# Optimization experiments

Hardware: AMD Instinct MI355X
Metric: run time of the kernel (lower is better)

## Reference

```python
import jax, jax.numpy as jnp
import numpy as np

WINDOW = 9       # attn_params.attention_window
DILATION = 1     # attn_params.attention_stride


def setup_inputs() -> dict:
    key = jax.random.key(0)
    kq, kk, kv = jax.random.split(key, 3)
    shape = (1, 8, 64, 64, 32)  # [B, heads, H, W, head_dim]
    return {
        "q": jax.random.normal(kq, shape, dtype=jnp.float32),
        "k": jax.random.normal(kk, shape, dtype=jnp.float32),
        "v": jax.random.normal(kv, shape, dtype=jnp.float32),
    }


def _neighborhood_attention_2d(q, k, v, K):
    """NATTEN-style 2D neighborhood attention, dilation=1, non-causal.

    Each query (i,j) attends to a KxK window of keys; at the borders the
    window is shifted (clamped) to stay fully inside the feature map,
    matching NATTEN semantics (no zero padding / masking).
    """
    B, h, H, W, D = q.shape
    half = K // 2
    # window start per row/col, clamped so the full window fits
    si = jnp.clip(jnp.arange(H) - half, 0, H - K)            # [H]
    sj = jnp.clip(jnp.arange(W) - half, 0, W - K)            # [W]
    ii = si[:, None] + jnp.arange(K)[None, :]                # [H, K]
    jj = sj[:, None] + jnp.arange(K)[None, :]                # [W, K]
    # gather neighborhoods: -> [B,h,H,K,W,K,D] -> [B,h,H,W,K,K,D]
    kn = jnp.transpose(k[:, :, ii][:, :, :, :, jj], (0, 1, 2, 4, 3, 5, 6))
    vn = jnp.transpose(v[:, :, ii][:, :, :, :, jj], (0, 1, 2, 4, 3, 5, 6))
    scale = 1.0 / jnp.sqrt(jnp.asarray(D, q.dtype))
    # logits over the KxK neighborhood
    logits = jnp.einsum('bhijd,bhijxyd->bhijxy', q * scale, kn)
    attn = jax.nn.softmax(logits.reshape(B, h, H, W, K * K), axis=-1)
    attn = attn.reshape(B, h, H, W, K, K)
    return jnp.einsum('bhijxy,bhijxyd->bhijd', attn, vn)


def reference(q, k, v):
    # mirror NA.forward: kernel_size = min(window, H, W), forced odd
    K = min(WINDOW, q.shape[2], q.shape[3])
    K -= 1 if K % 2 == 0 else 0
    return _neighborhood_attention_2d(q, k, v, K)
```

## Files before the change

kernel.cpp:

```cpp
#include <hip/hip_runtime.h>

#define HH 64
#define WW 64
#define DD 32
#define KW 9

typedef _Float16 f16;
typedef __attribute__((ext_vector_type(8))) _Float16 f16x8;
typedef __attribute__((ext_vector_type(4))) float f32x4;

__device__ __forceinline__ unsigned pk2(float lo, float hi) {
    unsigned short a = __builtin_bit_cast(unsigned short, (_Float16)lo);
    unsigned short b = __builtin_bit_cast(unsigned short, (_Float16)hi);
    return (unsigned)a | ((unsigned)b << 16);
}

__global__ __launch_bounds__(256) void na_attn_fused(
    const float* __restrict__ q, const float* __restrict__ k,
    const float* __restrict__ v, float* __restrict__ out)
{
    const int lane = threadIdx.x & 63;
    const int wv   = (blockIdx.x << 2) + (threadIdx.x >> 6);
    const int g    = lane >> 4;
    const int c16  = lane & 15;
    const int h  = wv >> 8;
    const int t  = wv & 255;
    const int i0 = (t >> 3) * 2;
    const int j0 = (t & 7) * 8;
    const int ry = min(max(i0 - 4, 0), HH - 10);
    const int rx = min(max(j0 - 4, 0), WW - 16);
    const int qi = i0 + (c16 >> 3);
    const int qj = j0 + (c16 & 7);
    const int si = min(max(qi - 4, 0), HH - KW);
    const int sj = min(max(qj - 4, 0), WW - KW);

    const int xb = rx + 4 * g;
    const bool cv0 = (unsigned)(xb + 0 - sj) < 9u;
    const bool cv1 = (unsigned)(xb + 1 - sj) < 9u;
    const bool cv2 = (unsigned)(xb + 2 - sj) < 9u;
    const bool cv3 = (unsigned)(xb + 3 - sj) < 9u;

    const float S = 0.17677669529663687f;
    const float* qp = q + (((size_t)h * HH + qi) * WW + qj) * DD + g * 8;
    f32x4 q0 = *(const f32x4*)qp;
    f32x4 q1 = *(const f32x4*)(qp + 4);
    union { unsigned u[4]; f16x8 h8; } Bq;
    Bq.u[0] = pk2(q0[0] * S, q0[1] * S);
    Bq.u[1] = pk2(q0[2] * S, q0[3] * S);
    Bq.u[2] = pk2(q1[0] * S, q1[1] * S);
    Bq.u[3] = pk2(q1[2] * S, q1[3] * S);

    const float* kbase = k + (((size_t)h * HH + ry) * WW + rx + c16) * DD + g * 8;
    const float* vbase = v + (((size_t)h * HH + (ry + (g >> 1))) * WW + rx + 8 * (g & 1)) * DD + c16;

    const int  sA  = c16 + ((g & 1) << 5);
    const int  sB  = sA + 16;
    const bool ghi = (g >= 2);

    f32x4 o0 = {0.f, 0.f, 0.f, 0.f};
    f32x4 o1 = {0.f, 0.f, 0.f, 0.f};
    const f32x4 zero = {0.f, 0.f, 0.f, 0.f};
    float lsum = 0.f;

#pragma unroll
    for (int cc = 0; cc < 5; ++cc) {
        const float* kp0 = kbase + (2 * cc) * (WW * DD);
        const float* kp1 = kp0 + (WW * DD);
        f32x4 ka = *(const f32x4*)kp0;
        f32x4 kb = *(const f32x4*)(kp0 + 4);
        f32x4 kc = *(const f32x4*)kp1;
        f32x4 kd = *(const f32x4*)(kp1 + 4);
        union { unsigned u[4]; f16x8 h8; } A0, A1;
        A0.u[0] = pk2(ka[0], ka[1]); A0.u[1] = pk2(ka[2], ka[3]);
        A0.u[2] = pk2(kb[0], kb[1]); A0.u[3] = pk2(kb[2], kb[3]);
        A1.u[0] = pk2(kc[0], kc[1]); A1.u[1] = pk2(kc[2], kc[3]);
        A1.u[2] = pk2(kd[0], kd[1]); A1.u[3] = pk2(kd[2], kd[3]);
        f32x4 s0 = __builtin_amdgcn_mfma_f32_16x16x32_f16(A0.h8, Bq.h8, zero, 0, 0, 0);
        f32x4 s1 = __builtin_amdgcn_mfma_f32_16x16x32_f16(A1.h8, Bq.h8, zero, 0, 0, 0);

        const bool rv0 = (unsigned)(ry + 2 * cc     - si) < 9u;
        const bool rv1 = (unsigned)(ry + 2 * cc + 1 - si) < 9u;
        const float p00 = (rv0 && cv0) ? __expf(s0[0]) : 0.f;
        const float p01 = (rv0 && cv1) ? __expf(s0[1]) : 0.f;
        const float p02 = (rv0 && cv2) ? __expf(s0[2]) : 0.f;
        const float p03 = (rv0 && cv3) ? __expf(s0[3]) : 0.f;
        const float p10 = (rv1 && cv0) ? __expf(s1[0]) : 0.f;
        const float p11 = (rv1 && cv1) ? __expf(s1[1]) : 0.f;
        const float p12 = (rv1 && cv2) ? __expf(s1[2]) : 0.f;
        const float p13 = (rv1 && cv3) ? __expf(s1[3]) : 0.f;
        lsum += ((p00 + p01) + (p02 + p03)) + ((p10 + p11) + (p12 + p13));

        const unsigned w0 = pk2(p00, p01);
        const unsigned w1 = pk2(p02, p03);
        const unsigned w2 = pk2(p10, p11);
        const unsigned w3 = pk2(p12, p13);
        const unsigned a0 = (unsigned)__shfl((int)w0, sA);
        const unsigned a1 = (unsigned)__shfl((int)w1, sA);
        const unsigned a2 = (unsigned)__shfl((int)w2, sA);
        const unsigned a3 = (unsigned)__shfl((int)w3, sA);
        const unsigned b0 = (unsigned)__shfl((int)w0, sB);
        const unsigned b1 = (unsigned)__shfl((int)w1, sB);
        const unsigned b2 = (unsigned)__shfl((int)w2, sB);
        const unsigned b3 = (unsigned)__shfl((int)w3, sB);
        union { unsigned u[4]; f16x8 h8; } bp;
        bp.u[0] = ghi ? a2 : a0;
        bp.u[1] = ghi ? a3 : a1;
        bp.u[2] = ghi ? b2 : b0;
        bp.u[3] = ghi ? b3 : b1;

        const float* vp = vbase + 2 * cc * (WW * DD);
        const float va0 = vp[0 * DD],      va1 = vp[1 * DD];
        const float va2 = vp[2 * DD],      va3 = vp[3 * DD];
        const float va4 = vp[4 * DD],      va5 = vp[5 * DD];
        const float va6 = vp[6 * DD],      va7 = vp[7 * DD];
        const float vb0 = vp[0 * DD + 16], vb1 = vp[1 * DD + 16];
        const float vb2 = vp[2 * DD + 16], vb3 = vp[3 * DD + 16];
        const float vb4 = vp[4 * DD + 16], vb5 = vp[5 * DD + 16];
        const float vb6 = vp[6 * DD + 16], vb7 = vp[7 * DD + 16];
        union { unsigned u[4]; f16x8 h8; } Av0, Av1;
        Av0.u[0] = pk2(va0, va1); Av0.u[1] = pk2(va2, va3);
        Av0.u[2] = pk2(va4, va5); Av0.u[3] = pk2(va6, va7);
        Av1.u[0] = pk2(vb0, vb1); Av1.u[1] = pk2(vb2, vb3);
        Av1.u[2] = pk2(vb4, vb5); Av1.u[3] = pk2(vb6, vb7);

        o0 = __builtin_amdgcn_mfma_f32_16x16x32_f16(Av0.h8, bp.h8, o0, 0, 0, 0);
        o1 = __builtin_amdgcn_mfma_f32_16x16x32_f16(Av1.h8, bp.h8, o1, 0, 0, 0);
    }

    lsum += __shfl_xor(lsum, 16);
    lsum += __shfl_xor(lsum, 32);
    const float inv = 1.0f / lsum;

    const int qid = (h << 12) + (qi << 6) + qj;
    float* ob = out + (size_t)qid * DD + 4 * g;
    f32x4 r0 = o0 * inv;
    f32x4 r1 = o1 * inv;
    *(f32x4*)(ob)      = r0;
    *(f32x4*)(ob + 16) = r1;
}

extern "C" void kernel_launch(void* const* d_in, const int* in_sizes, int n_in,
                              void* d_out, int out_size, void* d_ws, size_t ws_size,
                              hipStream_t stream) {
    const float* q = (const float*)d_in[0];
    const float* k = (const float*)d_in[1];
    const float* v = (const float*)d_in[2];
    float* out = (float*)d_out;

    na_attn_fused<<<512, 256, 0, stream>>>(q, k, v, out);
}
```

Before: 13.49 us.

## Split each tile's key-row chunks across two waves and merge via LDS

Each 16-query tile is now handled by two waves that each process three of the row-pair chunks (the second wave's last chunk is clamped and masked out). Partial outputs and softmax denominators from the second wave go through LDS and are summed by the first wave before normalisation and store. Loads for the next chunk are issued ahead of the compute for the current one, giving software pipelining. The change doubles the wave count and adds parallelism, at the cost of an LDS round trip, a block barrier and one redundant chunk of loads and MFMAs per tile.

```diff
diff --git a/kernel.cpp b/kernel.cpp
--- a/kernel.cpp
+++ b/kernel.cpp
@@ -15,14 +15,22 @@
     return (unsigned)a | ((unsigned)b << 16);
 }
 
-__global__ __launch_bounds__(256) void na_attn_fused(
+#define MFMA16(A, B, C) __builtin_amdgcn_mfma_f32_16x16x32_f16((A), (B), (C), 0, 0, 0)
+
+__global__ __launch_bounds__(256, 4) void na_attn_split(
     const float* __restrict__ q, const float* __restrict__ k,
     const float* __restrict__ v, float* __restrict__ out)
 {
-    const int lane = threadIdx.x & 63;
-    const int wv   = (blockIdx.x << 2) + (threadIdx.x >> 6);
-    const int g    = lane >> 4;
-    const int c16  = lane & 15;
+    __shared__ float lds[2][64][13];
+
+    const int lane  = threadIdx.x & 63;
+    const int wslot = threadIdx.x >> 6;
+    const int tpos  = wslot >> 1;
+    const int role  = wslot & 1;
+    const int wv    = (blockIdx.x << 1) + tpos;
+    const int g     = lane >> 4;
+    const int c16   = lane & 15;
+
     const int h  = wv >> 8;
     const int t  = wv & 255;
     const int i0 = (t >> 3) * 2;
@@ -50,8 +58,8 @@
     Bq.u[2] = pk2(q1[0] * S, q1[1] * S);
     Bq.u[3] = pk2(q1[2] * S, q1[3] * S);
 
-    const float* kbase = k + (((size_t)h * HH + ry) * WW + rx + c16) * DD + g * 8;
-    const float* vbase = v + (((size_t)h * HH + (ry + (g >> 1))) * WW + rx + 8 * (g & 1)) * DD + c16;
+    const float* kbase  = k + (((size_t)h * HH + ry) * WW + rx + c16) * DD + g * 8;
+    const float* vbase0 = v + (((size_t)h * HH + ry) * WW + rx + 8 * (g & 1)) * DD + c16;
 
     const int  sA  = c16 + ((g & 1) << 5);
     const int  sB  = sA + 16;
@@ -62,81 +70,109 @@
     const f32x4 zero = {0.f, 0.f, 0.f, 0.f};
     float lsum = 0.f;
 
-#pragma unroll
-    for (int cc = 0; cc < 5; ++cc) {
-        const float* kp0 = kbase + (2 * cc) * (WW * DD);
-        const float* kp1 = kp0 + (WW * DD);
-        f32x4 ka = *(const f32x4*)kp0;
-        f32x4 kb = *(const f32x4*)(kp0 + 4);
-        f32x4 kc = *(const f32x4*)kp1;
-        f32x4 kd = *(const f32x4*)(kp1 + 4);
-        union { unsigned u[4]; f16x8 h8; } A0, A1;
-        A0.u[0] = pk2(ka[0], ka[1]); A0.u[1] = pk2(ka[2], ka[3]);
-        A0.u[2] = pk2(kb[0], kb[1]); A0.u[3] = pk2(kb[2], kb[3]);
-        A1.u[0] = pk2(kc[0], kc[1]); A1.u[1] = pk2(kc[2], kc[3]);
-        A1.u[2] = pk2(kd[0], kd[1]); A1.u[3] = pk2(kd[2], kd[3]);
-        f32x4 s0 = __builtin_amdgcn_mfma_f32_16x16x32_f16(A0.h8, Bq.h8, zero, 0, 0, 0);
-        f32x4 s1 = __builtin_amdgcn_mfma_f32_16x16x32_f16(A1.h8, Bq.h8, zero, 0, 0, 0);
+    const int c0 = role * 3;
 
-        const bool rv0 = (unsigned)(ry + 2 * cc     - si) < 9u;
-        const bool rv1 = (unsigned)(ry + 2 * cc + 1 - si) < 9u;
-        const float p00 = (rv0 && cv0) ? __expf(s0[0]) : 0.f;
-        const float p01 = (rv0 && cv1) ? __expf(s0[1]) : 0.f;
-        const float p02 = (rv0 && cv2) ? __expf(s0[2]) : 0.f;
-        const float p03 = (rv0 && cv3) ? __expf(s0[3]) : 0.f;
-        const float p10 = (rv1 && cv0) ? __expf(s1[0]) : 0.f;
-        const float p11 = (rv1 && cv1) ? __expf(s1[1]) : 0.f;
-        const float p12 = (rv1 && cv2) ? __expf(s1[2]) : 0.f;
-        const float p13 = (rv1 && cv3) ? __expf(s1[3]) : 0.f;
-        lsum += ((p00 + p01) + (p02 + p03)) + ((p10 + p11) + (p12 + p13));
+#define LOADC(KA, KB, KC, KD, VA, VB, CIDX) do {                              \
+    const int rlo_ = min(2 * (CIDX), 9);                                      \
+    const int rhi_ = min(2 * (CIDX) + 1, 9);                                  \
+    const int vr_  = min(2 * (CIDX) + (g >> 1), 9);                           \
+    const float* kp0_ = kbase + rlo_ * (WW * DD);                             \
+    const float* kp1_ = kbase + rhi_ * (WW * DD);                             \
+    KA = *(const f32x4*)kp0_;  KB = *(const f32x4*)(kp0_ + 4);                \
+    KC = *(const f32x4*)kp1_;  KD = *(const f32x4*)(kp1_ + 4);                \
+    const float* vp_ = vbase0 + vr_ * (WW * DD);                              \
+    VA[0] = vp_[0 * DD];      VA[1] = vp_[1 * DD];                            \
+    VA[2] = vp_[2 * DD];      VA[3] = vp_[3 * DD];                            \
+    VA[4] = vp_[4 * DD];      VA[5] = vp_[5 * DD];                            \
+    VA[6] = vp_[6 * DD];      VA[7] = vp_[7 * DD];                            \
+    VB[0] = vp_[0 * DD + 16]; VB[1] = vp_[1 * DD + 16];                       \
+    VB[2] = vp_[2 * DD + 16]; VB[3] = vp_[3 * DD + 16];                       \
+    VB[4] = vp_[4 * DD + 16]; VB[5] = vp_[5 * DD + 16];                       \
+    VB[6] = vp_[6 * DD + 16]; VB[7] = vp_[7 * DD + 16];                       \
+} while (0)
 
-        const unsigned w0 = pk2(p00, p01);
-        const unsigned w1 = pk2(p02, p03);
-        const unsigned w2 = pk2(p10, p11);
-        const unsigned w3 = pk2(p12, p13);
-        const unsigned a0 = (unsigned)__shfl((int)w0, sA);
-        const unsigned a1 = (unsigned)__shfl((int)w1, sA);
-        const unsigned a2 = (unsigned)__shfl((int)w2, sA);
-        const unsigned a3 = (unsigned)__shfl((int)w3, sA);
-        const unsigned b0 = (unsigned)__shfl((int)w0, sB);
-        const unsigned b1 = (unsigned)__shfl((int)w1, sB);
-        const unsigned b2 = (unsigned)__shfl((int)w2, sB);
-        const unsigned b3 = (unsigned)__shfl((int)w3, sB);
-        union { unsigned u[4]; f16x8 h8; } bp;
-        bp.u[0] = ghi ? a2 : a0;
-        bp.u[1] = ghi ? a3 : a1;
-        bp.u[2] = ghi ? b2 : b0;
-        bp.u[3] = ghi ? b3 : b1;
+#define COMPC(KA, KB, KC, KD, VA, VB, CIDX) do {                              \
+    union { unsigned u[4]; f16x8 h8; } A0_, A1_;                              \
+    A0_.u[0] = pk2(KA[0], KA[1]); A0_.u[1] = pk2(KA[2], KA[3]);               \
+    A0_.u[2] = pk2(KB[0], KB[1]); A0_.u[3] = pk2(KB[2], KB[3]);               \
+    A1_.u[0] = pk2(KC[0], KC[1]); A1_.u[1] = pk2(KC[2], KC[3]);               \
+    A1_.u[2] = pk2(KD[0], KD[1]); A1_.u[3] = pk2(KD[2], KD[3]);               \
+    f32x4 s0_ = MFMA16(A0_.h8, Bq.h8, zero);                                  \
+    f32x4 s1_ = MFMA16(A1_.h8, Bq.h8, zero);                                  \
+    const bool rv0_ = (2 * (CIDX) < 10) &&                                    \
+                      ((unsigned)(ry + 2 * (CIDX) - si) < 9u);                \
+    const bool rv1_ = (2 * (CIDX) + 1 < 10) &&                                \
+                      ((unsigned)(ry + 2 * (CIDX) + 1 - si) < 9u);            \
+    const float p00_ = (rv0_ && cv0) ? __expf(s0_[0]) : 0.f;                  \
+    const float p01_ = (rv0_ && cv1) ? __expf(s0_[1]) : 0.f;                  \
+    const float p02_ = (rv0_ && cv2) ? __expf(s0_[2]) : 0.f;                  \
+    const float p03_ = (rv0_ && cv3) ? __expf(s0_[3]) : 0.f;                  \
+    const float p10_ = (rv1_ && cv0) ? __expf(s1_[0]) : 0.f;                  \
+    const float p11_ = (rv1_ && cv1) ? __expf(s1_[1]) : 0.f;                  \
+    const float p12_ = (rv1_ && cv2) ? __expf(s1_[2]) : 0.f;                  \
+    const float p13_ = (rv1_ && cv3) ? __expf(s1_[3]) : 0.f;                  \
+    lsum += ((p00_ + p01_) + (p02_ + p03_)) + ((p10_ + p11_) + (p12_ + p13_));\
+    const unsigned w0_ = pk2(p00_, p01_);                                     \
+    const unsigned w1_ = pk2(p02_, p03_);                                     \
+    const unsigned w2_ = pk2(p10_, p11_);                                     \
+    const unsigned w3_ = pk2(p12_, p13_);                                     \
+    const unsigned a0_ = (unsigned)__shfl((int)w0_, sA);                      \
+    const unsigned a1_ = (unsigned)__shfl((int)w1_, sA);                      \
+    const unsigned a2_ = (unsigned)__shfl((int)w2_, sA);                      \
+    const unsigned a3_ = (unsigned)__shfl((int)w3_, sA);                      \
+    const unsigned b0_ = (unsigned)__shfl((int)w0_, sB);                      \
+    const unsigned b1_ = (unsigned)__shfl((int)w1_, sB);                      \
+    const unsigned b2_ = (unsigned)__shfl((int)w2_, sB);                      \
+    const unsigned b3_ = (unsigned)__shfl((int)w3_, sB);                      \
+    union { unsigned u[4]; f16x8 h8; } bp_;                                   \
+    bp_.u[0] = ghi ? a2_ : a0_;                                               \
+    bp_.u[1] = ghi ? a3_ : a1_;                                               \
+    bp_.u[2] = ghi ? b2_ : b0_;                                               \
+    bp_.u[3] = ghi ? b3_ : b1_;                                               \
+    union { unsigned u[4]; f16x8 h8; } Av0_, Av1_;                            \
+    Av0_.u[0] = pk2(VA[0], VA[1]); Av0_.u[1] = pk2(VA[2], VA[3]);             \
+    Av0_.u[2] = pk2(VA[4], VA[5]); Av0_.u[3] = pk2(VA[6], VA[7]);             \
+    Av1_.u[0] = pk2(VB[0], VB[1]); Av1_.u[1] = pk2(VB[2], VB[3]);             \
+    Av1_.u[2] = pk2(VB[4], VB[5]); Av1_.u[3] = pk2(VB[6], VB[7]);             \
+    o0 = MFMA16(Av0_.h8, bp_.h8, o0);                                         \
+    o1 = MFMA16(Av1_.h8, bp_.h8, o1);                                         \
+} while (0)
 
-        const float* vp = vbase + 2 * cc * (WW * DD);
-        const float va0 = vp[0 * DD],      va1 = vp[1 * DD];
-        const float va2 = vp[2 * DD],      va3 = vp[3 * DD];
-        const float va4 = vp[4 * DD],      va5 = vp[5 * DD];
-        const float va6 = vp[6 * DD],      va7 = vp[7 * DD];
-        const float vb0 = vp[0 * DD + 16], vb1 = vp[1 * DD + 16];
-        const float vb2 = vp[2 * DD + 16], vb3 = vp[3 * DD + 16];
-        const float vb4 = vp[4 * DD + 16], vb5 = vp[5 * DD + 16];
-        const float vb6 = vp[6 * DD + 16], vb7 = vp[7 * DD + 16];
-        union { unsigned u[4]; f16x8 h8; } Av0, Av1;
-        Av0.u[0] = pk2(va0, va1); Av0.u[1] = pk2(va2, va3);
-        Av0.u[2] = pk2(va4, va5); Av0.u[3] = pk2(va6, va7);
-        Av1.u[0] = pk2(vb0, vb1); Av1.u[1] = pk2(vb2, vb3);
-        Av1.u[2] = pk2(vb4, vb5); Av1.u[3] = pk2(vb6, vb7);
+    f32x4 kA0, kB0, kC0, kD0, kA1, kB1, kC1, kD1;
+    float vA0[8], vB0[8], vA1[8], vB1[8];
 
-        o0 = __builtin_amdgcn_mfma_f32_16x16x32_f16(Av0.h8, bp.h8, o0, 0, 0, 0);
-        o1 = __builtin_amdgcn_mfma_f32_16x16x32_f16(Av1.h8, bp.h8, o1, 0, 0, 0);
-    }
+    LOADC(kA0, kB0, kC0, kD0, vA0, vB0, c0 + 0);
+    LOADC(kA1, kB1, kC1, kD1, vA1, vB1, c0 + 1);
+    COMPC(kA0, kB0, kC0, kD0, vA0, vB0, c0 + 0);
+    LOADC(kA0, kB0, kC0, kD0, vA0, vB0, c0 + 2);
+    COMPC(kA1, kB1, kC1, kD1, vA1, vB1, c0 + 1);
+    COMPC(kA0, kB0, kC0, kD0, vA0, vB0, c0 + 2);
 
     lsum += __shfl_xor(lsum, 16);
     lsum += __shfl_xor(lsum, 32);
-    const float inv = 1.0f / lsum;
 
-    const int qid = (h << 12) + (qi << 6) + qj;
-    float* ob = out + (size_t)qid * DD + 4 * g;
-    f32x4 r0 = o0 * inv;
-    f32x4 r1 = o1 * inv;
-    *(f32x4*)(ob)      = r0;
-    *(f32x4*)(ob + 16) = r1;
+    if (role == 1) {
+        float* p = lds[tpos][lane];
+        p[0] = o0[0]; p[1] = o0[1]; p[2] = o0[2]; p[3] = o0[3];
+        p[4] = o1[0]; p[5] = o1[1]; p[6] = o1[2]; p[7] = o1[3];
+        p[8] = lsum;
+    }
+    __syncthreads();
+    if (role == 0) {
+        const float* p = lds[tpos][lane];
+        o0[0] += p[0]; o0[1] += p[1]; o0[2] += p[2]; o0[3] += p[3];
+        o1[0] += p[4]; o1[1] += p[5]; o1[2] += p[6]; o1[3] += p[7];
+        lsum  += p[8];
+        const float inv = 1.0f / lsum;
+        const int qid = (h << 12) + (qi << 6) + qj;
+        float* ob = out + (size_t)qid * DD + 4 * g;
+        f32x4 r0 = o0 * inv;
+        f32x4 r1 = o1 * inv;
+        *(f32x4*)(ob)      = r0;
+        *(f32x4*)(ob + 16) = r1;
+    }
+#undef LOADC
+#undef COMPC
 }
 
 extern "C" void kernel_launch(void* const* d_in, const int* in_sizes, int n_in,
@@ -147,5 +183,5 @@
     const float* v = (const float*)d_in[2];
     float* out = (float*)d_out;
 
-    na_attn_fused<<<512, 256, 0, stream>>>(q, k, v, out);
+    na_attn_split<<<1024, 256, 0, stream>>>(q, k, v, out);
 }
```

New measurement: 16.03 us. 18.8% more time.

## Process four query rows per wave to reuse loaded K/V tiles

Applied to the files above, without the earlier changes.

Each wave now handles a 4x8 query tile instead of 2x8. It loads a 12-row K/V region once and runs score and PV MFMAs for two query row-pairs against it. This cuts redundant global loads and the fp32-to-fp16 conversion of K/V per query. In exchange the grid halves to 256 blocks, which lowers parallelism on a many-CU GPU, and each wave does more serial work with higher register pressure.

```diff
diff --git a/kernel.cpp b/kernel.cpp
--- a/kernel.cpp
+++ b/kernel.cpp
@@ -15,7 +15,9 @@
     return (unsigned)a | ((unsigned)b << 16);
 }
 
-__global__ __launch_bounds__(256) void na_attn_fused(
+#define MFMA16(A, B, C) __builtin_amdgcn_mfma_f32_16x16x32_f16((A), (B), (C), 0, 0, 0)
+
+__global__ __launch_bounds__(256) void na_attn_q4(
     const float* __restrict__ q, const float* __restrict__ k,
     const float* __restrict__ v, float* __restrict__ out)
 {
@@ -23,16 +25,19 @@
     const int wv   = (blockIdx.x << 2) + (threadIdx.x >> 6);
     const int g    = lane >> 4;
     const int c16  = lane & 15;
-    const int h  = wv >> 8;
-    const int t  = wv & 255;
-    const int i0 = (t >> 3) * 2;
+    const int h  = wv >> 7;
+    const int t  = wv & 127;
+    const int i0 = (t >> 3) * 4;
     const int j0 = (t & 7) * 8;
-    const int ry = min(max(i0 - 4, 0), HH - 10);
+    const int ry = min(max(i0 - 4, 0), HH - 12);
     const int rx = min(max(j0 - 4, 0), WW - 16);
-    const int qi = i0 + (c16 >> 3);
-    const int qj = j0 + (c16 & 7);
-    const int si = min(max(qi - 4, 0), HH - KW);
-    const int sj = min(max(qj - 4, 0), WW - KW);
+
+    const int qj  = j0 + (c16 & 7);
+    const int qiL = i0 + (c16 >> 3);
+    const int qiH = qiL + 2;
+    const int sj  = min(max(qj - 4, 0), WW - KW);
+    const int siL = min(max(qiL - 4, 0), HH - KW);
+    const int siH = min(max(qiH - 4, 0), HH - KW);
 
     const int xb = rx + 4 * g;
     const bool cv0 = (unsigned)(xb + 0 - sj) < 9u;
@@ -41,14 +46,21 @@
     const bool cv3 = (unsigned)(xb + 3 - sj) < 9u;
 
     const float S = 0.17677669529663687f;
-    const float* qp = q + (((size_t)h * HH + qi) * WW + qj) * DD + g * 8;
-    f32x4 q0 = *(const f32x4*)qp;
-    f32x4 q1 = *(const f32x4*)(qp + 4);
-    union { unsigned u[4]; f16x8 h8; } Bq;
-    Bq.u[0] = pk2(q0[0] * S, q0[1] * S);
-    Bq.u[1] = pk2(q0[2] * S, q0[3] * S);
-    Bq.u[2] = pk2(q1[0] * S, q1[1] * S);
-    Bq.u[3] = pk2(q1[2] * S, q1[3] * S);
+    const float* qpL = q + (((size_t)h * HH + qiL) * WW + qj) * DD + g * 8;
+    const float* qpH = q + (((size_t)h * HH + qiH) * WW + qj) * DD + g * 8;
+    f32x4 qa = *(const f32x4*)qpL;
+    f32x4 qb = *(const f32x4*)(qpL + 4);
+    f32x4 qc = *(const f32x4*)qpH;
+    f32x4 qd = *(const f32x4*)(qpH + 4);
+    union { unsigned u[4]; f16x8 h8; } BqL, BqH;
+    BqL.u[0] = pk2(qa[0] * S, qa[1] * S);
+    BqL.u[1] = pk2(qa[2] * S, qa[3] * S);
+    BqL.u[2] = pk2(qb[0] * S, qb[1] * S);
+    BqL.u[3] = pk2(qb[2] * S, qb[3] * S);
+    BqH.u[0] = pk2(qc[0] * S, qc[1] * S);
+    BqH.u[1] = pk2(qc[2] * S, qc[3] * S);
+    BqH.u[2] = pk2(qd[0] * S, qd[1] * S);
+    BqH.u[3] = pk2(qd[2] * S, qd[3] * S);
 
     const float* kbase = k + (((size_t)h * HH + ry) * WW + rx + c16) * DD + g * 8;
     const float* vbase = v + (((size_t)h * HH + (ry + (g >> 1))) * WW + rx + 8 * (g & 1)) * DD + c16;
@@ -57,13 +69,15 @@
     const int  sB  = sA + 16;
     const bool ghi = (g >= 2);
 
-    f32x4 o0 = {0.f, 0.f, 0.f, 0.f};
-    f32x4 o1 = {0.f, 0.f, 0.f, 0.f};
+    f32x4 oL0 = {0.f, 0.f, 0.f, 0.f};
+    f32x4 oL1 = {0.f, 0.f, 0.f, 0.f};
+    f32x4 oH0 = {0.f, 0.f, 0.f, 0.f};
+    f32x4 oH1 = {0.f, 0.f, 0.f, 0.f};
     const f32x4 zero = {0.f, 0.f, 0.f, 0.f};
-    float lsum = 0.f;
+    float lsumL = 0.f, lsumH = 0.f;
 
 #pragma unroll
-    for (int cc = 0; cc < 5; ++cc) {
+    for (int cc = 0; cc < 6; ++cc) {
         const float* kp0 = kbase + (2 * cc) * (WW * DD);
         const float* kp1 = kp0 + (WW * DD);
         f32x4 ka = *(const f32x4*)kp0;
@@ -75,38 +89,6 @@
         A0.u[2] = pk2(kb[0], kb[1]); A0.u[3] = pk2(kb[2], kb[3]);
         A1.u[0] = pk2(kc[0], kc[1]); A1.u[1] = pk2(kc[2], kc[3]);
         A1.u[2] = pk2(kd[0], kd[1]); A1.u[3] = pk2(kd[2], kd[3]);
-        f32x4 s0 = __builtin_amdgcn_mfma_f32_16x16x32_f16(A0.h8, Bq.h8, zero, 0, 0, 0);
-        f32x4 s1 = __builtin_amdgcn_mfma_f32_16x16x32_f16(A1.h8, Bq.h8, zero, 0, 0, 0);
-
-        const bool rv0 = (unsigned)(ry + 2 * cc     - si) < 9u;
-        const bool rv1 = (unsigned)(ry + 2 * cc + 1 - si) < 9u;
-        const float p00 = (rv0 && cv0) ? __expf(s0[0]) : 0.f;
-        const float p01 = (rv0 && cv1) ? __expf(s0[1]) : 0.f;
-        const float p02 = (rv0 && cv2) ? __expf(s0[2]) : 0.f;
-        const float p03 = (rv0 && cv3) ? __expf(s0[3]) : 0.f;
-        const float p10 = (rv1 && cv0) ? __expf(s1[0]) : 0.f;
-        const float p11 = (rv1 && cv1) ? __expf(s1[1]) : 0.f;
-        const float p12 = (rv1 && cv2) ? __expf(s1[2]) : 0.f;
-        const float p13 = (rv1 && cv3) ? __expf(s1[3]) : 0.f;
-        lsum += ((p00 + p01) + (p02 + p03)) + ((p10 + p11) + (p12 + p13));
-
-        const unsigned w0 = pk2(p00, p01);
-        const unsigned w1 = pk2(p02, p03);
-        const unsigned w2 = pk2(p10, p11);
-        const unsigned w3 = pk2(p12, p13);
-        const unsigned a0 = (unsigned)__shfl((int)w0, sA);
-        const unsigned a1 = (unsigned)__shfl((int)w1, sA);
-        const unsigned a2 = (unsigned)__shfl((int)w2, sA);
-        const unsigned a3 = (unsigned)__shfl((int)w3, sA);
-        const unsigned b0 = (unsigned)__shfl((int)w0, sB);
-        const unsigned b1 = (unsigned)__shfl((int)w1, sB);
-        const unsigned b2 = (unsigned)__shfl((int)w2, sB);
-        const unsigned b3 = (unsigned)__shfl((int)w3, sB);
-        union { unsigned u[4]; f16x8 h8; } bp;
-        bp.u[0] = ghi ? a2 : a0;
-        bp.u[1] = ghi ? a3 : a1;
-        bp.u[2] = ghi ? b2 : b0;
-        bp.u[3] = ghi ? b3 : b1;
 
         const float* vp = vbase + 2 * cc * (WW * DD);
         const float va0 = vp[0 * DD],      va1 = vp[1 * DD];
@@ -123,20 +105,96 @@
         Av1.u[0] = pk2(vb0, vb1); Av1.u[1] = pk2(vb2, vb3);
         Av1.u[2] = pk2(vb4, vb5); Av1.u[3] = pk2(vb6, vb7);
 
-        o0 = __builtin_amdgcn_mfma_f32_16x16x32_f16(Av0.h8, bp.h8, o0, 0, 0, 0);
-        o1 = __builtin_amdgcn_mfma_f32_16x16x32_f16(Av1.h8, bp.h8, o1, 0, 0, 0);
+        f32x4 sL0 = MFMA16(A0.h8, BqL.h8, zero);
+        f32x4 sL1 = MFMA16(A1.h8, BqL.h8, zero);
+        f32x4 sH0 = MFMA16(A0.h8, BqH.h8, zero);
+        f32x4 sH1 = MFMA16(A1.h8, BqH.h8, zero);
+
+        const int r0 = ry + 2 * cc, r1 = r0 + 1;
+        const bool rvL0 = (unsigned)(r0 - siL) < 9u;
+        const bool rvL1 = (unsigned)(r1 - siL) < 9u;
+        const bool rvH0 = (unsigned)(r0 - siH) < 9u;
+        const bool rvH1 = (unsigned)(r1 - siH) < 9u;
+
+        const float pL00 = (rvL0 && cv0) ? __expf(sL0[0]) : 0.f;
+        const float pL01 = (rvL0 && cv1) ? __expf(sL0[1]) : 0.f;
+        const float pL02 = (rvL0 && cv2) ? __expf(sL0[2]) : 0.f;
+        const float pL03 = (rvL0 && cv3) ? __expf(sL0[3]) : 0.f;
+        const float pL10 = (rvL1 && cv0) ? __expf(sL1[0]) : 0.f;
+        const float pL11 = (rvL1 && cv1) ? __expf(sL1[1]) : 0.f;
+        const float pL12 = (rvL1 && cv2) ? __expf(sL1[2]) : 0.f;
+        const float pL13 = (rvL1 && cv3) ? __expf(sL1[3]) : 0.f;
+        lsumL += ((pL00 + pL01) + (pL02 + pL03)) + ((pL10 + pL11) + (pL12 + pL13));
+
+        const float pH00 = (rvH0 && cv0) ? __expf(sH0[0]) : 0.f;
+        const float pH01 = (rvH0 && cv1) ? __expf(sH0[1]) : 0.f;
+        const float pH02 = (rvH0 && cv2) ? __expf(sH0[2]) : 0.f;
+        const float pH03 = (rvH0 && cv3) ? __expf(sH0[3]) : 0.f;
+        const float pH10 = (rvH1 && cv0) ? __expf(sH1[0]) : 0.f;
+        const float pH11 = (rvH1 && cv1) ? __expf(sH1[1]) : 0.f;
+        const float pH12 = (rvH1 && cv2) ? __expf(sH1[2]) : 0.f;
+        const float pH13 = (rvH1 && cv3) ? __expf(sH1[3]) : 0.f;
+        lsumH += ((pH00 + pH01) + (pH02 + pH03)) + ((pH10 + pH11) + (pH12 + pH13));
+
+        {
+            const unsigned w0 = pk2(pL00, pL01);
+            const unsigned w1 = pk2(pL02, pL03);
+            const unsigned w2 = pk2(pL10, pL11);
+            const unsigned w3 = pk2(pL12, pL13);
+            const unsigned a0 = (unsigned)__shfl((int)w0, sA);
+            const unsigned a1 = (unsigned)__shfl((int)w1, sA);
+            const unsigned a2 = (unsigned)__shfl((int)w2, sA);
+            const unsigned a3 = (unsigned)__shfl((int)w3, sA);
+            const unsigned b0 = (unsigned)__shfl((int)w0, sB);
+            const unsigned b1 = (unsigned)__shfl((int)w1, sB);
+            const unsigned b2 = (unsigned)__shfl((int)w2, sB);
+            const unsigned b3 = (unsigned)__shfl((int)w3, sB);
+            union { unsigned u[4]; f16x8 h8; } bp;
+            bp.u[0] = ghi ? a2 : a0;
+            bp.u[1] = ghi ? a3 : a1;
+            bp.u[2] = ghi ? b2 : b0;
+            bp.u[3] = ghi ? b3 : b1;
+            oL0 = MFMA16(Av0.h8, bp.h8, oL0);
+            oL1 = MFMA16(Av1.h8, bp.h8, oL1);
+        }
+        {
+            const unsigned w0 = pk2(pH00, pH01);
+            const unsigned w1 = pk2(pH02, pH03);
+            const unsigned w2 = pk2(pH10, pH11);
+            const unsigned w3 = pk2(pH12, pH13);
+            const unsigned a0 = (unsigned)__shfl((int)w0, sA);
+            const unsigned a1 = (unsigned)__shfl((int)w1, sA);
+            const unsigned a2 = (unsigned)__shfl((int)w2, sA);
+            const unsigned a3 = (unsigned)__shfl((int)w3, sA);
+            const unsigned b0 = (unsigned)__shfl((int)w0, sB);
+            const unsigned b1 = (unsigned)__shfl((int)w1, sB);
+            const unsigned b2 = (unsigned)__shfl((int)w2, sB);
+            const unsigned b3 = (unsigned)__shfl((int)w3, sB);
+            union { unsigned u[4]; f16x8 h8; } bp;
+            bp.u[0] = ghi ? a2 : a0;
+            bp.u[1] = ghi ? a3 : a1;
+            bp.u[2] = ghi ? b2 : b0;
+            bp.u[3] = ghi ? b3 : b1;
+            oH0 = MFMA16(Av0.h8, bp.h8, oH0);
+            oH1 = MFMA16(Av1.h8, bp.h8, oH1);
+        }
     }
 
-    lsum += __shfl_xor(lsum, 16);
-    lsum += __shfl_xor(lsum, 32);
-    const float inv = 1.0f / lsum;
-
-    const int qid = (h << 12) + (qi << 6) + qj;
-    float* ob = out + (size_t)qid * DD + 4 * g;
-    f32x4 r0 = o0 * inv;
-    f32x4 r1 = o1 * inv;
-    *(f32x4*)(ob)      = r0;
-    *(f32x4*)(ob + 16) = r1;
+    lsumL += __shfl_xor(lsumL, 16);
+    lsumL += __shfl_xor(lsumL, 32);
+    lsumH += __shfl_xor(lsumH, 16);
+    lsumH += __shfl_xor(lsumH, 32);
+    const float invL = 1.0f / lsumL;
+    const float invH = 1.0f / lsumH;
+
+    const int qidL = (h << 12) + (qiL << 6) + qj;
+    const int qidH = (h << 12) + (qiH << 6) + qj;
+    float* obL = out + (size_t)qidL * DD + 4 * g;
+    float* obH = out + (size_t)qidH * DD + 4 * g;
+    *(f32x4*)(obL)      = oL0 * invL;
+    *(f32x4*)(obL + 16) = oL1 * invL;
+    *(f32x4*)(obH)      = oH0 * invH;
+    *(f32x4*)(obH + 16) = oH1 * invH;
 }
 
 extern "C" void kernel_launch(void* const* d_in, const int* in_sizes, int n_in,
@@ -147,5 +205,5 @@
     const float* v = (const float*)d_in[2];
     float* out = (float*)d_out;
 
-    na_attn_fused<<<512, 256, 0, stream>>>(q, k, v, out);
+    na_attn_q4<<<256, 256, 0, stream>>>(q, k, v, out);
 }
```

Result: faster. 11.99 us (-11.1%).
